# Kernel tuning notes

Measured on AMD Instinct MI355X. Metric: run time of the kernel, lower is better.

Reference implementation:

```python
import jax, jax.numpy as jnp
import numpy as np

N = 50000   # nodes
E = 200000  # edges (avg degree ~4, pose-graph-like sparsity)
F_IN = 512
NEG_SLOPE = 0.01  # F.leaky_relu default


def _softmax_aggr(src_feat, dst, num_nodes):
    # torch_geometric SoftmaxAggregation(t=1): per-destination, per-feature
    # alpha = softmax(x_j), out = sum_j alpha * x_j
    m = jax.ops.segment_max(src_feat, dst, num_segments=num_nodes)  # [N,F]
    m = jnp.where(jnp.isfinite(m), m, 0.0)  # empty segments -> -inf guard
    e = jnp.exp(src_feat - m[dst])                                   # [E,F]
    denom = jax.ops.segment_sum(e, dst, num_segments=num_nodes)      # [N,F]
    num = jax.ops.segment_sum(e * src_feat, dst, num_segments=num_nodes)
    return num / jnp.maximum(denom, 1e-16)  # 0 for isolated nodes


def setup_inputs() -> dict:
    key = jax.random.key(0)
    ks = jax.random.split(key, 9)
    inp = {
        "x": jax.random.normal(ks[0], (N, F_IN), dtype=jnp.float32),
        "W1_rel": jax.random.normal(ks[1], (513, 256), dtype=jnp.float32) * 0.04,
        "b1_rel": jnp.zeros((256,), dtype=jnp.float32),
        "W1_root": jax.random.normal(ks[2], (513, 256), dtype=jnp.float32) * 0.04,
        "W2_rel": jax.random.normal(ks[3], (257, 64), dtype=jnp.float32) * 0.06,
        "b2_rel": jnp.zeros((64,), dtype=jnp.float32),
        "W2_root": jax.random.normal(ks[4], (257, 64), dtype=jnp.float32) * 0.06,
        "Wp": jax.random.normal(ks[5], (65, 3), dtype=jnp.float32) * 0.1,
        "bp": jnp.zeros((3,), dtype=jnp.float32),
        "Wr": jax.random.normal(ks[6], (65, 4), dtype=jnp.float32) * 0.1,
        "br": jnp.zeros((4,), dtype=jnp.float32),
        "edge_index": jax.random.randint(ks[7], (2, E), 0, N, dtype=jnp.int64),
    }
    return inp


def reference(x, W1_rel, b1_rel, W1_root, W2_rel, b2_rel, W2_root,
              Wp, bp, Wr, br, edge_index):
    src, dst = edge_index[0], edge_index[1]
    node_index = jnp.arange(x.shape[0], dtype=x.dtype)[:, None]  # [N,1]

    # dropout is identity in eval mode
    h = jnp.concatenate([x, node_index], axis=1)  # [N,513]

    # GraphConv(513,256, aggr='softmax'): lin_rel(softmax_aggr(x_j)) + lin_root(x)
    agg1 = _softmax_aggr(h[src], dst, x.shape[0])               # [N,513]
    h = agg1 @ W1_rel + b1_rel + h @ W1_root                     # [N,256]
    h = jnp.where(h >= 0, h, NEG_SLOPE * h)

    h = jnp.concatenate([h, node_index], axis=1)  # [N,257]

    # GraphConv(257,64) default aggr='add'
    agg2 = jax.ops.segment_sum(h[src], dst, num_segments=x.shape[0])  # [N,257]
    h = agg2 @ W2_rel + b2_rel + h @ W2_root                           # [N,64]
    h = jnp.where(h >= 0, h, NEG_SLOPE * h)

    h = jnp.concatenate([h, node_index], axis=1)  # [N,65]

    position = h @ Wp + bp                         # [N,3]
    rotation = h @ Wr + br                         # [N,4]
    norm = jnp.linalg.norm(rotation, axis=1, keepdims=True)
    rotation = rotation / jnp.maximum(norm, 1e-12)  # F.normalize

    return jnp.concatenate([position, rotation], axis=1)  # [N,7]
```

## Files before the change

### kernel.cpp

```cpp
#include <hip/hip_runtime.h>

#define NNODES 50000
#define NEDGES 200000
#define NSCANB ((NNODES + 255) / 256)

typedef short  bf16x8 __attribute__((ext_vector_type(8)));
typedef float  f32x4  __attribute__((ext_vector_type(4)));
typedef unsigned int u32x4 __attribute__((ext_vector_type(4)));

__device__ __forceinline__ unsigned short f2bf(float f) {
    union { float f; unsigned int u; } c; c.f = f;
    unsigned int r = c.u + 0x7fffu + ((c.u >> 16) & 1u);
    return (unsigned short)(r >> 16);
}
__device__ __forceinline__ float bf2f(unsigned short h) {
    union { unsigned int u; float f; } c; c.u = ((unsigned int)h) << 16;
    return c.f;
}
__device__ __forceinline__ float bflo(unsigned int v) {
    union { unsigned int u; float f; } c; c.u = v << 16;
    return c.f;
}
__device__ __forceinline__ float bfhi(unsigned int v) {
    union { unsigned int u; float f; } c; c.u = v & 0xffff0000u;
    return c.f;
}

#define PREP_B1 (256 * 1024)
#define PREP_B2 (128 * 256)
#define PREP_XC (NNODES * 64)
__global__ __launch_bounds__(256) void k_prepcount(const float* __restrict__ x,
                                                   const float* __restrict__ W1_rel,
                                                   const float* __restrict__ W1_root,
                                                   const float* __restrict__ W2_rel,
                                                   const float* __restrict__ W2_root,
                                                   const int* __restrict__ ei,
                                                   int* __restrict__ deg,
                                                   unsigned short* __restrict__ Bt1,
                                                   unsigned short* __restrict__ Bt2,
                                                   unsigned short* __restrict__ xb) {
    const int gtid = blockIdx.x * 256 + threadIdx.x;
    const int GS = gridDim.x * 256;
    for (int e = gtid; e < NEDGES; e += GS) atomicAdd(&deg[ei[NEDGES + e]], 1);
    for (int i = gtid; i < PREP_B1; i += GS) {
        int n = i >> 10, k = i & 1023;
        float v = (k < 512) ? W1_rel[k * 256 + n] : W1_root[(k - 512) * 256 + n];
        Bt1[i] = f2bf(v);
    }
    for (int i = gtid; i < PREP_B2; i += GS) {
        int n = i >> 8, k = i & 255;
        float v = (n < 64) ? W2_rel[k * 64 + n] : W2_root[k * 64 + (n - 64)];
        Bt2[i] = f2bf(v);
    }
    for (int i = gtid; i < PREP_XC; i += GS) {
        int n = i >> 6, c8 = (i & 63) * 8;
        const float* xp = x + (size_t)n * 512 + c8;
        float4 a = *(const float4*)xp;
        float4 bb = *(const float4*)(xp + 4);
        unsigned short o[8];
        o[0] = f2bf(a.x); o[1] = f2bf(a.y); o[2] = f2bf(a.z); o[3] = f2bf(a.w);
        o[4] = f2bf(bb.x); o[5] = f2bf(bb.y); o[6] = f2bf(bb.z); o[7] = f2bf(bb.w);
        *(u32x4*)(xb + (size_t)n * 512 + c8) = *(const u32x4*)o;
    }
}

__global__ __launch_bounds__(256) void k_scanA(const int* __restrict__ deg,
                                               int* __restrict__ rs,
                                               int* __restrict__ partials) {
    __shared__ int sm[256];
    int t = threadIdx.x, i = blockIdx.x * 256 + t;
    int v = (i < NNODES) ? deg[i] : 0;
    sm[t] = v;
    __syncthreads();
#pragma unroll
    for (int off = 1; off < 256; off <<= 1) {
        int u = (t >= off) ? sm[t - off] : 0;
        __syncthreads();
        sm[t] += u;
        __syncthreads();
    }
    if (i < NNODES) rs[i] = sm[t] - v;
    if (t == 255) partials[blockIdx.x] = sm[255];
}

__global__ __launch_bounds__(256) void k_scanC2(int* __restrict__ rs,
                                                const int* __restrict__ partials,
                                                int* __restrict__ cursor) {
    __shared__ int sm[256];
    int t = threadIdx.x, b = blockIdx.x;
    sm[t] = (t < b && t < NSCANB) ? partials[t] : 0;
    __syncthreads();
#pragma unroll
    for (int off = 128; off; off >>= 1) {
        if (t < off) sm[t] += sm[t + off];
        __syncthreads();
    }
    int off0 = sm[0];
    int i = b * 256 + t;
    if (i < NNODES) {
        int rv = rs[i] + off0;
        rs[i] = rv;
        cursor[i] = rv;
    }
    if (i == 0) rs[NNODES] = NEDGES;
}

__global__ void k_scatter(const int* __restrict__ ei, int* __restrict__ cursor,
                          int* __restrict__ srcs) {
    int e = blockIdx.x * 256 + threadIdx.x;
    if (e < NEDGES) {
        int d = ei[NEDGES + e];
        int p = atomicAdd(&cursor[d], 1);
        srcs[p] = ei[e];
    }
}

__global__ __launch_bounds__(256) void k_agg1(const unsigned short* __restrict__ xb,
                                              const int* __restrict__ rs,
                                              const int* __restrict__ srcs,
                                              unsigned short* __restrict__ AggBuf) {
    int wv = threadIdx.x >> 6;
    int lane = threadIdx.x & 63;
    int n = blockIdx.x * 4 + wv;
    int e0 = rs[n], e1 = rs[n + 1];
    float nu[8], de[8];
#pragma unroll
    for (int j = 0; j < 8; ++j) { nu[j] = 0.f; de[j] = 0.f; }

    auto accum = [&](u32x4 r) {
#pragma unroll
        for (int p = 0; p < 4; ++p) {
            float v0 = bflo(r[p]), v1 = bfhi(r[p]);
            float E0 = __expf(v0), E1 = __expf(v1);
            de[2 * p] += E0; nu[2 * p] += E0 * v0;
            de[2 * p + 1] += E1; nu[2 * p + 1] += E1 * v1;
        }
    };

    int e = e0;
    for (; e + 3 < e1; e += 4) {
        int s0 = srcs[e], s1 = srcs[e + 1], s2 = srcs[e + 2], s3 = srcs[e + 3];
        u32x4 r0 = *(const u32x4*)(xb + (size_t)s0 * 512 + lane * 8);
        u32x4 r1 = *(const u32x4*)(xb + (size_t)s1 * 512 + lane * 8);
        u32x4 r2 = *(const u32x4*)(xb + (size_t)s2 * 512 + lane * 8);
        u32x4 r3 = *(const u32x4*)(xb + (size_t)s3 * 512 + lane * 8);
        accum(r0); accum(r1); accum(r2); accum(r3);
    }
    if (e + 1 < e1) {
        int s0 = srcs[e], s1 = srcs[e + 1];
        u32x4 r0 = *(const u32x4*)(xb + (size_t)s0 * 512 + lane * 8);
        u32x4 r1 = *(const u32x4*)(xb + (size_t)s1 * 512 + lane * 8);
        accum(r0); accum(r1);
        e += 2;
    }
    if (e < e1) {
        u32x4 r0 = *(const u32x4*)(xb + (size_t)srcs[e] * 512 + lane * 8);
        accum(r0);
    }
    unsigned short o[8];
#pragma unroll
    for (int j = 0; j < 8; ++j) o[j] = f2bf(nu[j] / fmaxf(de[j], 1e-16f));
    *(u32x4*)(AggBuf + (size_t)n * 512 + lane * 8) = *(const u32x4*)o;
}

__global__ __launch_bounds__(256) void k_gemm1(const unsigned short* __restrict__ A1,
                                               const unsigned short* __restrict__ A2,
                                               const unsigned short* __restrict__ Bt,
                                               const int* __restrict__ rs,
                                               const int* __restrict__ srcs,
                                               const float* __restrict__ r1,
                                               const float* __restrict__ r2,
                                               const float* __restrict__ bias,
                                               unsigned short* __restrict__ outp) {
    constexpr int BM = 64, BN = 128, BK = 64;
    __shared__ __align__(16) unsigned short As[2][BM * BK];
    __shared__ __align__(16) unsigned short Bs[2][BN * BK];
    __shared__ float s1t[BM];

    const int tid = threadIdx.x;
    const int w = tid >> 6;
    const int lane = tid & 63;
    const int lm = lane & 15;
    const int quad = lane >> 4;
    const int wr = w >> 1;
    const int wc = w & 1;
    const int rowbase = blockIdx.y * BM;
    const int colbase = blockIdx.x * BN;
    const int wrow = wr * 32;
    const int wcol = wc * 64;

    const int rsub = lane >> 3;
    const int csw = (lane & 7) ^ rsub;

    f32x4 acc[2][4];
#pragma unroll
    for (int mi = 0; mi < 2; ++mi)
#pragma unroll
        for (int ni = 0; ni < 4; ++ni) acc[mi][ni] = (f32x4){0.f, 0.f, 0.f, 0.f};

    auto stage = [&](unsigned short* Asb, unsigned short* Bsb, int kt) {
        const unsigned short* Ab = (kt < 512) ? A1 : A2;
        int kof = (kt < 512) ? kt : kt - 512;
#pragma unroll
        for (int l = 0; l < 2; ++l) {
            int r = w * 16 + l * 8;
            int gr = rowbase + r + rsub;
            if (gr >= NNODES) gr = NNODES - 1;
            const unsigned short* gp = Ab + (size_t)gr * 512 + kof + csw * 8;
            __builtin_amdgcn_global_load_lds(
                (const __attribute__((address_space(1))) void*)gp,
                (__attribute__((address_space(3))) void*)(Asb + r * BK), 16, 0, 0);
        }
#pragma unroll
        for (int l = 0; l < 4; ++l) {
            int r = w * 32 + l * 8;
            const unsigned short* gp = Bt + (size_t)(colbase + r + rsub) * 1024 + kt + csw * 8;
            __builtin_amdgcn_global_load_lds(
                (const __attribute__((address_space(1))) void*)gp,
                (__attribute__((address_space(3))) void*)(Bsb + r * BK), 16, 0, 0);
        }
    };

    auto compute = [&](const unsigned short* Asb, const unsigned short* Bsb) {
#pragma unroll
        for (int kk = 0; kk < BK; kk += 32) {
            const int kidx = (kk >> 3) + quad;
            const int phys = kidx ^ (lm & 7);
            bf16x8 af[2], bfr[4];
#pragma unroll
            for (int mi = 0; mi < 2; ++mi)
                af[mi] = __builtin_bit_cast(bf16x8,
                    *(const u32x4*)(Asb + (wrow + mi * 16 + lm) * BK + phys * 8));
#pragma unroll
            for (int ni = 0; ni < 4; ++ni)
                bfr[ni] = __builtin_bit_cast(bf16x8,
                    *(const u32x4*)(Bsb + (wcol + ni * 16 + lm) * BK + phys * 8));
#pragma unroll
            for (int mi = 0; mi < 2; ++mi)
#pragma unroll
                for (int ni = 0; ni < 4; ++ni)
                    acc[mi][ni] = __builtin_amdgcn_mfma_f32_16x16x32_bf16(
                        af[mi], bfr[ni], acc[mi][ni], 0, 0, 0);
        }
    };

    stage(As[0], Bs[0], 0);
#pragma unroll 1
    for (int t = 0; t < 16; t += 2) {
        stage(As[1], Bs[1], (t + 1) * BK);
        asm volatile("s_waitcnt vmcnt(6)" ::: "memory");
        __builtin_amdgcn_s_barrier();
        __builtin_amdgcn_sched_barrier(0);
        compute(As[0], Bs[0]);
        __builtin_amdgcn_s_barrier();
        if (t + 2 < 16) {
            stage(As[0], Bs[0], (t + 2) * BK);
            asm volatile("s_waitcnt vmcnt(6)" ::: "memory");
        } else {
            asm volatile("s_waitcnt vmcnt(0)" ::: "memory");
        }
        __builtin_amdgcn_s_barrier();
        __builtin_amdgcn_sched_barrier(0);
        compute(As[1], Bs[1]);
        __builtin_amdgcn_s_barrier();
    }

    if (tid < BM) {
        int grow = rowbase + tid;
        float r_ = 0.f;
        if (grow < NNODES) {
            int e0 = rs[grow], e1 = rs[grow + 1];
            float m = -INFINITY, d = 0.f, q = 0.f;
            for (int e = e0; e < e1; ++e) {
                float v = (float)srcs[e];
                float nm = fmaxf(m, v);
                float sc = __expf(m - nm), ee = __expf(v - nm);
                d = d * sc + ee;
                q = q * sc + ee * v;
                m = nm;
            }
            r_ = q / fmaxf(d, 1e-16f);
        }
        s1t[tid] = r_;
    }
    __syncthreads();

#pragma unroll
    for (int ni = 0; ni < 4; ++ni) {
        int gc = colbase + wcol + ni * 16 + lm;
        float r1v = r1[gc], r2v = r2[gc], bv = bias[gc];
#pragma unroll
        for (int mi = 0; mi < 2; ++mi) {
#pragma unroll
            for (int r = 0; r < 4; ++r) {
                int lrow = wrow + mi * 16 + quad * 4 + r;
                int grow = rowbase + lrow;
                if (grow < NNODES) {
                    float v = acc[mi][ni][r] + s1t[lrow] * r1v + (float)grow * r2v + bv;
                    v = (v >= 0.f) ? v : 0.01f * v;
                    outp[(size_t)grow * 256 + gc] = f2bf(v);
                }
            }
        }
    }
}

__global__ __launch_bounds__(256) void k_gemm2(const unsigned short* __restrict__ H1,
                                               const unsigned short* __restrict__ Bt,
                                               unsigned short* __restrict__ GR) {
    constexpr int BM = 64, BN = 128, BK = 64;
    __shared__ __align__(16) unsigned short As[BM * BK];
    __shared__ __align__(16) unsigned short Bs[BN * BK];

    const int tid = threadIdx.x;
    const int w = tid >> 6;
    const int lane = tid & 63;
    const int lm = lane & 15;
    const int quad = lane >> 4;
    const int wr = w >> 1;
    const int wc = w & 1;
    const int rowbase = blockIdx.x * BM;
    const int wrow = wr * 32;
    const int wcol = wc * 64;

    const int rsub = lane >> 3;
    const int csw = (lane & 7) ^ rsub;

    f32x4 acc[2][4];
#pragma unroll
    for (int mi = 0; mi < 2; ++mi)
#pragma unroll
        for (int ni = 0; ni < 4; ++ni) acc[mi][ni] = (f32x4){0.f, 0.f, 0.f, 0.f};

#pragma unroll 1
    for (int kt = 0; kt < 256; kt += BK) {
#pragma unroll
        for (int l = 0; l < 2; ++l) {
            int r = w * 16 + l * 8;
            int gr = rowbase + r + rsub;
            if (gr >= NNODES) gr = NNODES - 1;
            const unsigned short* gp = H1 + (size_t)gr * 256 + kt + csw * 8;
            __builtin_amdgcn_global_load_lds(
                (const __attribute__((address_space(1))) void*)gp,
                (__attribute__((address_space(3))) void*)(As + r * BK), 16, 0, 0);
        }
#pragma unroll
        for (int l = 0; l < 4; ++l) {
            int r = w * 32 + l * 8;
            const unsigned short* gp = Bt + (size_t)(r + rsub) * 256 + kt + csw * 8;
            __builtin_amdgcn_global_load_lds(
                (const __attribute__((address_space(1))) void*)gp,
                (__attribute__((address_space(3))) void*)(Bs + r * BK), 16, 0, 0);
        }
        __syncthreads();
#pragma unroll
        for (int kk = 0; kk < BK; kk += 32) {
            const int kidx = (kk >> 3) + quad;
            const int phys = kidx ^ (lm & 7);
            bf16x8 af[2], bfr[4];
#pragma unroll
            for (int mi = 0; mi < 2; ++mi)
                af[mi] = __builtin_bit_cast(bf16x8,
                    *(const u32x4*)(As + (wrow + mi * 16 + lm) * BK + phys * 8));
#pragma unroll
            for (int ni = 0; ni < 4; ++ni)
                bfr[ni] = __builtin_bit_cast(bf16x8,
                    *(const u32x4*)(Bs + (wcol + ni * 16 + lm) * BK + phys * 8));
#pragma unroll
            for (int mi = 0; mi < 2; ++mi)
#pragma unroll
                for (int ni = 0; ni < 4; ++ni)
                    acc[mi][ni] = __builtin_amdgcn_mfma_f32_16x16x32_bf16(
                        af[mi], bfr[ni], acc[mi][ni], 0, 0, 0);
        }
        __syncthreads();
    }

#pragma unroll
    for (int ni = 0; ni < 4; ++ni) {
        int gc = wcol + ni * 16 + lm;
#pragma unroll
        for (int mi = 0; mi < 2; ++mi) {
#pragma unroll
            for (int r = 0; r < 4; ++r) {
                int lrow = wrow + mi * 16 + quad * 4 + r;
                int grow = rowbase + lrow;
                if (grow < NNODES)
                    GR[(size_t)grow * 128 + gc] = f2bf(acc[mi][ni][r]);
            }
        }
    }
}

__global__ __launch_bounds__(256) void k_agg2h(const int* __restrict__ rs,
                                               const int* __restrict__ srcs,
                                               const unsigned short* __restrict__ GR,
                                               const float* __restrict__ r1,
                                               const float* __restrict__ r2,
                                               const float* __restrict__ bias,
                                               const float* __restrict__ Wp,
                                               const float* __restrict__ bp,
                                               const float* __restrict__ Wr,
                                               const float* __restrict__ br,
                                               float* __restrict__ out) {
    const int wv = threadIdx.x >> 6;
    const int lane = threadIdx.x & 63;
    const int n = blockIdx.x * 4 + wv;
    const int e0 = rs[n], e1 = rs[n + 1];

    float g = 0.f, si = 0.f;
    int e = e0;
    for (; e + 3 < e1; e += 4) {
        int s0 = srcs[e], s1 = srcs[e + 1], s2 = srcs[e + 2], s3 = srcs[e + 3];
        float g0 = bf2f(GR[(size_t)s0 * 128 + lane]);
        float g1 = bf2f(GR[(size_t)s1 * 128 + lane]);
        float g2 = bf2f(GR[(size_t)s2 * 128 + lane]);
        float g3 = bf2f(GR[(size_t)s3 * 128 + lane]);
        g += (g0 + g1) + (g2 + g3);
        si += (float)(s0 + s1) + (float)(s2 + s3);
    }
    if (e + 1 < e1) {
        int s0 = srcs[e], s1 = srcs[e + 1];
        g += bf2f(GR[(size_t)s0 * 128 + lane]) + bf2f(GR[(size_t)s1 * 128 + lane]);
        si += (float)(s0 + s1);
        e += 2;
    }
    if (e < e1) {
        int s0 = srcs[e];
        g += bf2f(GR[(size_t)s0 * 128 + lane]);
        si += (float)s0;
    }

    float h2 = g + si * r1[lane] + bf2f(GR[(size_t)n * 128 + 64 + lane])
             + (float)n * r2[lane] + bias[lane];
    h2 = (h2 >= 0.f) ? h2 : 0.01f * h2;

    float p0 = h2 * Wp[lane * 3 + 0];
    float p1 = h2 * Wp[lane * 3 + 1];
    float p2 = h2 * Wp[lane * 3 + 2];
    float q0 = h2 * Wr[lane * 4 + 0];
    float q1 = h2 * Wr[lane * 4 + 1];
    float q2 = h2 * Wr[lane * 4 + 2];
    float q3 = h2 * Wr[lane * 4 + 3];
#pragma unroll
    for (int m = 1; m < 64; m <<= 1) {
        p0 += __shfl_xor(p0, m);
        p1 += __shfl_xor(p1, m);
        p2 += __shfl_xor(p2, m);
        q0 += __shfl_xor(q0, m);
        q1 += __shfl_xor(q1, m);
        q2 += __shfl_xor(q2, m);
        q3 += __shfl_xor(q3, m);
    }
    const float idx = (float)n;
    p0 += idx * Wp[64 * 3 + 0] + bp[0];
    p1 += idx * Wp[64 * 3 + 1] + bp[1];
    p2 += idx * Wp[64 * 3 + 2] + bp[2];
    q0 += idx * Wr[64 * 4 + 0] + br[0];
    q1 += idx * Wr[64 * 4 + 1] + br[1];
    q2 += idx * Wr[64 * 4 + 2] + br[2];
    q3 += idx * Wr[64 * 4 + 3] + br[3];
    float nrm = fmaxf(sqrtf(q0 * q0 + q1 * q1 + q2 * q2 + q3 * q3), 1e-12f);
    float o = (lane == 0) ? p0 : (lane == 1) ? p1 : (lane == 2) ? p2
            : (lane == 3) ? q0 / nrm : (lane == 4) ? q1 / nrm
            : (lane == 5) ? q2 / nrm : q3 / nrm;
    if (lane < 7) out[(size_t)n * 7 + lane] = o;
}

extern "C" void kernel_launch(void* const* d_in, const int* in_sizes, int n_in,
                              void* d_out, int out_size, void* d_ws, size_t ws_size,
                              hipStream_t stream) {
    const float* x       = (const float*)d_in[0];
    const float* W1_rel  = (const float*)d_in[1];
    const float* b1      = (const float*)d_in[2];
    const float* W1_root = (const float*)d_in[3];
    const float* W2_rel  = (const float*)d_in[4];
    const float* b2      = (const float*)d_in[5];
    const float* W2_root = (const float*)d_in[6];
    const float* Wp      = (const float*)d_in[7];
    const float* bp      = (const float*)d_in[8];
    const float* Wr      = (const float*)d_in[9];
    const float* br      = (const float*)d_in[10];
    const int*   ei      = (const int*)d_in[11];
    float* out = (float*)d_out;

    char* ws = (char*)d_ws;
    size_t off = 0;
    auto alloc = [&](size_t bytes) {
        size_t o = off;
        off = (off + bytes + 255) & ~(size_t)255;
        return (void*)(ws + o);
    };
    int*   deg       = (int*)alloc(NNODES * 4);
    int*   cursor    = (int*)alloc(NNODES * 4);
    int*   row_start = (int*)alloc((NNODES + 1) * 4);
    int*   srcs      = (int*)alloc(NEDGES * 4);
    int*   partials  = (int*)alloc(NSCANB * 4);
    unsigned short* xb     = (unsigned short*)alloc((size_t)NNODES * 512 * 2);
    unsigned short* AggBuf = (unsigned short*)alloc((size_t)NNODES * 512 * 2);
    unsigned short* H1     = (unsigned short*)alloc((size_t)NNODES * 256 * 2);
    unsigned short* GR     = (unsigned short*)alloc((size_t)NNODES * 128 * 2);
    unsigned short* Bt1    = (unsigned short*)alloc(256 * 1024 * 2);
    unsigned short* Bt2    = (unsigned short*)alloc(128 * 256 * 2);

    hipMemsetAsync(deg, 0, NNODES * 4, stream);

    k_prepcount<<<2048, 256, 0, stream>>>(
        x, W1_rel, W1_root, W2_rel, W2_root, ei, deg, Bt1, Bt2, xb);

    k_scanA<<<NSCANB, 256, 0, stream>>>(deg, row_start, partials);
    k_scanC2<<<NSCANB, 256, 0, stream>>>(row_start, partials, cursor);
    k_scatter<<<(NEDGES + 255) / 256, 256, 0, stream>>>(ei, cursor, srcs);

    k_agg1<<<NNODES / 4, 256, 0, stream>>>(xb, row_start, srcs, AggBuf);

    k_gemm1<<<dim3(2, (NNODES + 63) / 64), 256, 0, stream>>>(
        AggBuf, xb, Bt1, row_start, srcs, W1_rel + 512 * 256, W1_root + 512 * 256, b1, H1);

    k_gemm2<<<(NNODES + 63) / 64, 256, 0, stream>>>(H1, Bt2, GR);

    k_agg2h<<<NNODES / 4, 256, 0, stream>>>(
        row_start, srcs, GR, W2_rel + 256 * 64, W2_root + 256 * 64, b2,
        Wp, bp, Wr, br, out);
}
```

Before: 335.8 us.

## Fuse layer-1 and layer-2 GEMMs into one kernel with H1 kept in LDS

Merges k_gemm1 and k_gemm2 into a single 512-thread kernel in which each block computes the full 256-column H1 tile. The tile stays in swizzled LDS and is used directly as the A operand of the second GEMM. This drops the H1 global write and re-read, one kernel launch, and the duplicated A loads caused by the earlier 2-way column split. In exchange it uses 80KB of LDS per block, which limits occupancy, and the single-buffered second GEMM adds barriers.

```diff
diff --git a/kernel.cpp b/kernel.cpp
--- a/kernel.cpp
+++ b/kernel.cpp
@@ -163,32 +163,36 @@
     *(u32x4*)(AggBuf + (size_t)n * 512 + lane * 8) = *(const u32x4*)o;
 }
 
-__global__ __launch_bounds__(256) void k_gemm1(const unsigned short* __restrict__ A1,
-                                               const unsigned short* __restrict__ A2,
-                                               const unsigned short* __restrict__ Bt,
-                                               const int* __restrict__ rs,
-                                               const int* __restrict__ srcs,
-                                               const float* __restrict__ r1,
-                                               const float* __restrict__ r2,
-                                               const float* __restrict__ bias,
-                                               unsigned short* __restrict__ outp) {
-    constexpr int BM = 64, BN = 128, BK = 64;
-    __shared__ __align__(16) unsigned short As[2][BM * BK];
-    __shared__ __align__(16) unsigned short Bs[2][BN * BK];
-    __shared__ float s1t[BM];
+__global__ __launch_bounds__(512) void k_gemm12(const unsigned short* __restrict__ A1,
+                                                const unsigned short* __restrict__ A2,
+                                                const unsigned short* __restrict__ Bt,
+                                                const unsigned short* __restrict__ Bt2,
+                                                const int* __restrict__ rs,
+                                                const int* __restrict__ srcs,
+                                                const float* __restrict__ r1,
+                                                const float* __restrict__ r2,
+                                                const float* __restrict__ bias,
+                                                unsigned short* __restrict__ GR) {
+    constexpr int BM = 64, BK = 64;
+    __shared__ __align__(16) unsigned char lds_raw[81920];
+    unsigned short* AsB[2] = {(unsigned short*)(lds_raw),
+                              (unsigned short*)(lds_raw + 8192)};
+    unsigned short* BsB[2] = {(unsigned short*)(lds_raw + 16384),
+                              (unsigned short*)(lds_raw + 49152)};
+    unsigned short* h1t = (unsigned short*)(lds_raw);
+    unsigned short* B2s = (unsigned short*)(lds_raw + 32768);
+    float* s1t = (float*)(lds_raw + 49152);
 
     const int tid = threadIdx.x;
     const int w = tid >> 6;
     const int lane = tid & 63;
     const int lm = lane & 15;
     const int quad = lane >> 4;
-    const int wr = w >> 1;
-    const int wc = w & 1;
-    const int rowbase = blockIdx.y * BM;
-    const int colbase = blockIdx.x * BN;
+    const int wr = w >> 2;
+    const int wc = w & 3;
+    const int rowbase = blockIdx.x * BM;
     const int wrow = wr * 32;
     const int wcol = wc * 64;
-
     const int rsub = lane >> 3;
     const int csw = (lane & 7) ^ rsub;
 
@@ -201,9 +205,8 @@
     auto stage = [&](unsigned short* Asb, unsigned short* Bsb, int kt) {
         const unsigned short* Ab = (kt < 512) ? A1 : A2;
         int kof = (kt < 512) ? kt : kt - 512;
-#pragma unroll
-        for (int l = 0; l < 2; ++l) {
-            int r = w * 16 + l * 8;
+        {
+            int r = w * 8;
             int gr = rowbase + r + rsub;
             if (gr >= NNODES) gr = NNODES - 1;
             const unsigned short* gp = Ab + (size_t)gr * 512 + kof + csw * 8;
@@ -214,7 +217,7 @@
 #pragma unroll
         for (int l = 0; l < 4; ++l) {
             int r = w * 32 + l * 8;
-            const unsigned short* gp = Bt + (size_t)(colbase + r + rsub) * 1024 + kt + csw * 8;
+            const unsigned short* gp = Bt + (size_t)(r + rsub) * 1024 + kt + csw * 8;
             __builtin_amdgcn_global_load_lds(
                 (const __attribute__((address_space(1))) void*)gp,
                 (__attribute__((address_space(3))) void*)(Bsb + r * BK), 16, 0, 0);
@@ -244,24 +247,24 @@
         }
     };
 
-    stage(As[0], Bs[0], 0);
+    stage(AsB[0], BsB[0], 0);
 #pragma unroll 1
     for (int t = 0; t < 16; t += 2) {
-        stage(As[1], Bs[1], (t + 1) * BK);
-        asm volatile("s_waitcnt vmcnt(6)" ::: "memory");
+        stage(AsB[1], BsB[1], (t + 1) * BK);
+        asm volatile("s_waitcnt vmcnt(5)" ::: "memory");
         __builtin_amdgcn_s_barrier();
         __builtin_amdgcn_sched_barrier(0);
-        compute(As[0], Bs[0]);
+        compute(AsB[0], BsB[0]);
         __builtin_amdgcn_s_barrier();
         if (t + 2 < 16) {
-            stage(As[0], Bs[0], (t + 2) * BK);
-            asm volatile("s_waitcnt vmcnt(6)" ::: "memory");
+            stage(AsB[0], BsB[0], (t + 2) * BK);
+            asm volatile("s_waitcnt vmcnt(5)" ::: "memory");
         } else {
             asm volatile("s_waitcnt vmcnt(0)" ::: "memory");
         }
         __builtin_amdgcn_s_barrier();
         __builtin_amdgcn_sched_barrier(0);
-        compute(As[1], Bs[1]);
+        compute(AsB[1], BsB[1]);
         __builtin_amdgcn_s_barrier();
     }
 
@@ -287,106 +290,76 @@
 
 #pragma unroll
     for (int ni = 0; ni < 4; ++ni) {
-        int gc = colbase + wcol + ni * 16 + lm;
-        float r1v = r1[gc], r2v = r2[gc], bv = bias[gc];
+        int c = wcol + ni * 16 + lm;
+        float r1v = r1[c], r2v = r2[c], bv = bias[c];
 #pragma unroll
         for (int mi = 0; mi < 2; ++mi) {
 #pragma unroll
             for (int r = 0; r < 4; ++r) {
                 int lrow = wrow + mi * 16 + quad * 4 + r;
                 int grow = rowbase + lrow;
-                if (grow < NNODES) {
-                    float v = acc[mi][ni][r] + s1t[lrow] * r1v + (float)grow * r2v + bv;
-                    v = (v >= 0.f) ? v : 0.01f * v;
-                    outp[(size_t)grow * 256 + gc] = f2bf(v);
-                }
+                float v = acc[mi][ni][r] + s1t[lrow] * r1v + (float)grow * r2v + bv;
+                v = (v >= 0.f) ? v : 0.01f * v;
+                int pos = lrow * 256 + (((c >> 3) ^ (lrow & 7)) << 3) + (c & 7);
+                h1t[pos] = f2bf(v);
             }
         }
     }
-}
-
-__global__ __launch_bounds__(256) void k_gemm2(const unsigned short* __restrict__ H1,
-                                               const unsigned short* __restrict__ Bt,
-                                               unsigned short* __restrict__ GR) {
-    constexpr int BM = 64, BN = 128, BK = 64;
-    __shared__ __align__(16) unsigned short As[BM * BK];
-    __shared__ __align__(16) unsigned short Bs[BN * BK];
-
-    const int tid = threadIdx.x;
-    const int w = tid >> 6;
-    const int lane = tid & 63;
-    const int lm = lane & 15;
-    const int quad = lane >> 4;
-    const int wr = w >> 1;
-    const int wc = w & 1;
-    const int rowbase = blockIdx.x * BM;
-    const int wrow = wr * 32;
-    const int wcol = wc * 64;
-
-    const int rsub = lane >> 3;
-    const int csw = (lane & 7) ^ rsub;
-
-    f32x4 acc[2][4];
+    __syncthreads();
+
+    const int wr2 = w >> 2, wc2 = w & 3;
+    f32x4 acc2[2][2];
 #pragma unroll
     for (int mi = 0; mi < 2; ++mi)
 #pragma unroll
-        for (int ni = 0; ni < 4; ++ni) acc[mi][ni] = (f32x4){0.f, 0.f, 0.f, 0.f};
+        for (int ni = 0; ni < 2; ++ni) acc2[mi][ni] = (f32x4){0.f, 0.f, 0.f, 0.f};
 
 #pragma unroll 1
-    for (int kt = 0; kt < 256; kt += BK) {
+    for (int kt = 0; kt < 256; kt += 64) {
 #pragma unroll
         for (int l = 0; l < 2; ++l) {
             int r = w * 16 + l * 8;
-            int gr = rowbase + r + rsub;
-            if (gr >= NNODES) gr = NNODES - 1;
-            const unsigned short* gp = H1 + (size_t)gr * 256 + kt + csw * 8;
+            const unsigned short* gp = Bt2 + (size_t)(r + rsub) * 256 + kt + csw * 8;
             __builtin_amdgcn_global_load_lds(
                 (const __attribute__((address_space(1))) void*)gp,
-                (__attribute__((address_space(3))) void*)(As + r * BK), 16, 0, 0);
-        }
-#pragma unroll
-        for (int l = 0; l < 4; ++l) {
-            int r = w * 32 + l * 8;
-            const unsigned short* gp = Bt + (size_t)(r + rsub) * 256 + kt + csw * 8;
-            __builtin_amdgcn_global_load_lds(
-                (const __attribute__((address_space(1))) void*)gp,
-                (__attribute__((address_space(3))) void*)(Bs + r * BK), 16, 0, 0);
+                (__attribute__((address_space(3))) void*)(B2s + r * 64), 16, 0, 0);
         }
         __syncthreads();
 #pragma unroll
-        for (int kk = 0; kk < BK; kk += 32) {
+        for (int kk = 0; kk < 64; kk += 32) {
             const int kidx = (kk >> 3) + quad;
-            const int phys = kidx ^ (lm & 7);
-            bf16x8 af[2], bfr[4];
+            const int physB = kidx ^ (lm & 7);
+            const int cbg = (kt >> 3) + kidx;
+            const int physA = cbg ^ (lm & 7);
+            bf16x8 af[2], bfr[2];
 #pragma unroll
             for (int mi = 0; mi < 2; ++mi)
                 af[mi] = __builtin_bit_cast(bf16x8,
-                    *(const u32x4*)(As + (wrow + mi * 16 + lm) * BK + phys * 8));
-#pragma unroll
-            for (int ni = 0; ni < 4; ++ni)
+                    *(const u32x4*)(h1t + (wr2 * 32 + mi * 16 + lm) * 256 + physA * 8));
+#pragma unroll
+            for (int ni = 0; ni < 2; ++ni)
                 bfr[ni] = __builtin_bit_cast(bf16x8,
-                    *(const u32x4*)(Bs + (wcol + ni * 16 + lm) * BK + phys * 8));
+                    *(const u32x4*)(B2s + (wc2 * 32 + ni * 16 + lm) * 64 + physB * 8));
 #pragma unroll
             for (int mi = 0; mi < 2; ++mi)
 #pragma unroll
-                for (int ni = 0; ni < 4; ++ni)
-                    acc[mi][ni] = __builtin_amdgcn_mfma_f32_16x16x32_bf16(
-                        af[mi], bfr[ni], acc[mi][ni], 0, 0, 0);
+                for (int ni = 0; ni < 2; ++ni)
+                    acc2[mi][ni] = __builtin_amdgcn_mfma_f32_16x16x32_bf16(
+                        af[mi], bfr[ni], acc2[mi][ni], 0, 0, 0);
         }
         __syncthreads();
     }
 
 #pragma unroll
-    for (int ni = 0; ni < 4; ++ni) {
-        int gc = wcol + ni * 16 + lm;
+    for (int ni = 0; ni < 2; ++ni) {
+        int gc = wc2 * 32 + ni * 16 + lm;
 #pragma unroll
         for (int mi = 0; mi < 2; ++mi) {
 #pragma unroll
             for (int r = 0; r < 4; ++r) {
-                int lrow = wrow + mi * 16 + quad * 4 + r;
-                int grow = rowbase + lrow;
+                int grow = rowbase + wr2 * 32 + mi * 16 + quad * 4 + r;
                 if (grow < NNODES)
-                    GR[(size_t)grow * 128 + gc] = f2bf(acc[mi][ni][r]);
+                    GR[(size_t)grow * 128 + gc] = f2bf(acc2[mi][ni][r]);
             }
         }
     }
@@ -498,7 +471,6 @@
     int*   partials  = (int*)alloc(NSCANB * 4);
     unsigned short* xb     = (unsigned short*)alloc((size_t)NNODES * 512 * 2);
     unsigned short* AggBuf = (unsigned short*)alloc((size_t)NNODES * 512 * 2);
-    unsigned short* H1     = (unsigned short*)alloc((size_t)NNODES * 256 * 2);
     unsigned short* GR     = (unsigned short*)alloc((size_t)NNODES * 128 * 2);
     unsigned short* Bt1    = (unsigned short*)alloc(256 * 1024 * 2);
     unsigned short* Bt2    = (unsigned short*)alloc(128 * 256 * 2);
@@ -514,10 +486,9 @@
 
     k_agg1<<<NNODES / 4, 256, 0, stream>>>(xb, row_start, srcs, AggBuf);
 
-    k_gemm1<<<dim3(2, (NNODES + 63) / 64), 256, 0, stream>>>(
-        AggBuf, xb, Bt1, row_start, srcs, W1_rel + 512 * 256, W1_root + 512 * 256, b1, H1);
-
-    k_gemm2<<<(NNODES + 63) / 64, 256, 0, stream>>>(H1, Bt2, GR);
+    k_gemm12<<<(NNODES + 63) / 64, 512, 0, stream>>>(
+        AggBuf, xb, Bt1, Bt2, row_start, srcs,
+        W1_rel + 512 * 256, W1_root + 512 * 256, b1, GR);
 
     k_agg2h<<<NNODES / 4, 256, 0, stream>>>(
         row_start, srcs, GR, W2_rel + 256 * 64, W2_root + 256 * 64, b2,
```

Measured after the change: 321.2 us. 1.05x faster.
